# Performance work log

Measured on AMD Instinct MI355X. Metric: run time of the kernel, lower is better.

Reference implementation:

```python
import math
import jax, jax.numpy as jnp
import numpy as np

N, T, F, H = 30000, 4, 128, 8  # num_node, num_type, num_fea, num_head
D = F // H


def setup_inputs() -> dict:
    key = jax.random.key(0)
    k0, k1, k2, k3, k4 = jax.random.split(key, 5)
    feature = jax.random.normal(k0, (N, F), dtype=jnp.float32)
    edge_fea = jax.random.normal(k1, (N, T, F), dtype=jnp.float32)
    node_multi_mask = jax.random.randint(k2, (N,), 0, T)
    # Xavier-uniform-like scale for [*, F, F] projection tables
    xav = math.sqrt(6.0 / (F + F))
    node_proj = jax.random.uniform(k3, (T, F, F), minval=-xav, maxval=xav, dtype=jnp.float32)
    edge_proj = jax.random.uniform(k4, (T * T, F, F), minval=-xav, maxval=xav, dtype=jnp.float32)
    return {
        "feature": feature,
        "edge_fea": edge_fea,
        "node_multi_mask": node_multi_mask,
        "node_proj": node_proj,
        "edge_proj": edge_proj,
    }


def reference(feature, edge_fea, node_multi_mask, node_proj, edge_proj):
    # Type-indexed projections. Instead of gathering per-node [F,F] matrices
    # (which would materialize N*F*F), compute projections for all T source
    # types in one batched einsum, then select each node's type with a gather.
    # node: out[n] = node_proj[mask[n]] @ feature[n]
    node_all = jnp.einsum('tgf,nf->ntg', node_proj, feature)           # [N,T,F]
    node_p = jnp.take_along_axis(node_all, node_multi_mask[:, None, None], axis=1)[:, 0]  # [N,F]
    # edge: out[n,j] = edge_proj[mask[n]*T + j] @ edge_fea[n,j]
    edge_proj_r = edge_proj.reshape(T, T, F, F)                         # [src_type, j, F, F]
    edge_all = jnp.einsum('stgf,ntf->nstg', edge_proj_r, edge_fea)      # [N,T_src,T,F]
    edge_p = jnp.take_along_axis(edge_all, node_multi_mask[:, None, None, None], axis=1)[:, 0]  # [N,T,F]

    # multi-head attention weights
    node_multi_in = node_p.reshape(N, 1, H, D).transpose(0, 2, 1, 3) / math.sqrt(D)  # [N,H,1,D]
    edge_multi_in = edge_p.reshape(N, T, H, D).transpose(0, 2, 3, 1)                  # [N,H,D,T]
    scores = jnp.matmul(node_multi_in, edge_multi_in)                                 # [N,H,1,T]
    # NOTE: original uses nn.Softmax(dim=1) -> softmax over the HEAD axis
    all_r_weight = jax.nn.softmax(scores, axis=1).transpose(0, 3, 1, 2)               # [N,T,H,1]
    return all_r_weight
```

## Files before the change

### kernel.cpp

```cpp
#include <hip/hip_runtime.h>
#include <hip/hip_bf16.h>

#define N_NODES 30000
#define T_TYPES 4
#define F_DIM   128
#define H_HEADS 8

typedef __bf16 bf16x8 __attribute__((ext_vector_type(8)));
typedef __bf16 bf16x4 __attribute__((ext_vector_type(4)));
typedef float  floatx4 __attribute__((ext_vector_type(4)));

#define WS_REORDER 64
#define WS_NPB     480256
#define WS_EPB     611328

template <int CTRL>
static __device__ __forceinline__ float dpp_add(float x) {
    int xi = __builtin_bit_cast(int, x);
    int yi = __builtin_amdgcn_update_dpp(xi, xi, CTRL, 0xF, 0xF, true);
    return x + __builtin_bit_cast(float, yi);
}
static __device__ __forceinline__ float sum16(float x) {
    x = dpp_add<0xB1>(x);
    x = dpp_add<0x4E>(x);
    x = dpp_add<0x141>(x);
    x = dpp_add<0x140>(x);
    return x;
}

__global__ __launch_bounds__(256) void prep_kernel(
    const float* __restrict__ node_proj, const float* __restrict__ edge_proj,
    __bf16* __restrict__ npb, __bf16* __restrict__ epb, int* __restrict__ counts)
{
    int i = blockIdx.x * 256 + threadIdx.x;
    if (i < 4) counts[i] = 0;
    int base = i * 4;
    float4 v;
    __bf16* dst;
    if (base < T_TYPES * F_DIM * F_DIM) {
        v = ((const float4*)node_proj)[i];
        dst = npb + base;
    } else {
        int off = base - T_TYPES * F_DIM * F_DIM;
        v = ((const float4*)edge_proj)[off >> 2];
        dst = epb + off;
    }
    bf16x4 w = { (__bf16)v.x, (__bf16)v.y, (__bf16)v.z, (__bf16)v.w };
    *(bf16x4*)dst = w;
}

__global__ __launch_bounds__(256) void bucket_kernel(
    const int* __restrict__ mask, int* __restrict__ counts, int* __restrict__ reorder)
{
    int n = blockIdx.x * 256 + threadIdx.x;
    int lane = threadIdx.x & 63;
    int t = (n < N_NODES) ? mask[n] : -1;
    #pragma unroll
    for (int tt = 0; tt < T_TYPES; ++tt) {
        unsigned long long b = __ballot(t == tt);
        if (b == 0ull) continue;
        int cnt = __popcll(b);
        int leader = __ffsll((unsigned long long)b) - 1;
        int base = 0;
        if (lane == leader) base = atomicAdd(&counts[tt], cnt);
        base = __shfl(base, leader);
        if (t == tt) {
            int prefix = __popcll(b & ((1ull << lane) - 1ull));
            reorder[tt * N_NODES + base + prefix] = n;
        }
    }
}

__global__ __launch_bounds__(512) void main_kernel(
    const float* __restrict__ feature, const float* __restrict__ edge_fea,
    const int* __restrict__ counts, const int* __restrict__ reorder,
    const __bf16* __restrict__ npb, const __bf16* __restrict__ epb,
    float* __restrict__ out)
{
    const int b = blockIdx.x;
    const int t = b & 3;
    const int start = (b >> 2) * 32;
    const int Nt = counts[t];
    if (start >= Nt) return;
    const int valid = min(32, Nt - start);

    __shared__ __bf16 Afeat[32][136];
    __shared__ __bf16 Aedge[4][32][136];
    __shared__ float  sc[32][4][H_HEADS];
    __shared__ int    nidx[32];

    const int tid = threadIdx.x;
    if (tid < 32) {
        int s = (tid < valid) ? tid : (valid - 1);
        nidx[tid] = reorder[t * N_NODES + start + s];
    }
    __syncthreads();

    const int colv = tid & 31;
    const int rowg = tid >> 5;
    #pragma unroll
    for (int it = 0; it < 2; ++it) {
        int row = it * 16 + rowg;
        float4 v = ((const float4*)(feature + (long)nidx[row] * F_DIM))[colv];
        bf16x4 w = { (__bf16)v.x, (__bf16)v.y, (__bf16)v.z, (__bf16)v.w };
        *(bf16x4*)(&Afeat[row][0] + colv * 4) = w;
    }
    #pragma unroll
    for (int it = 0; it < 8; ++it) {
        int row = it * 16 + rowg;
        int j = row >> 5, r = row & 31;
        float4 v = ((const float4*)(edge_fea + ((long)nidx[r] * 4 + j) * F_DIM))[colv];
        bf16x4 w = { (__bf16)v.x, (__bf16)v.y, (__bf16)v.z, (__bf16)v.w };
        *(bf16x4*)(&Aedge[j][r][0] + colv * 4) = w;
    }
    __syncthreads();

    const int lane = tid & 63;
    const int wave = tid >> 6;
    const int ml   = lane & 15;
    const int quad = lane >> 4;
    const int g0   = wave * 16;

    floatx4 accN[2] = {};
    {
        const __bf16* a0 = &Afeat[ml][quad * 8];
        const __bf16* a1 = &Afeat[16 + ml][quad * 8];
        const __bf16* b0 = npb + t * (F_DIM * F_DIM) + (g0 + ml) * F_DIM + quad * 8;
        #pragma unroll
        for (int k0 = 0; k0 < 128; k0 += 32) {
            bf16x8 A0 = *(const bf16x8*)(a0 + k0);
            bf16x8 A1 = *(const bf16x8*)(a1 + k0);
            bf16x8 B0 = *(const bf16x8*)(b0 + k0);
            accN[0] = __builtin_amdgcn_mfma_f32_16x16x32_bf16(A0, B0, accN[0], 0, 0, 0);
            accN[1] = __builtin_amdgcn_mfma_f32_16x16x32_bf16(A1, B0, accN[1], 0, 0, 0);
        }
    }

    #pragma unroll
    for (int j = 0; j < 4; ++j) {
        floatx4 accE[2] = {};
        const __bf16* a0 = &Aedge[j][ml][quad * 8];
        const __bf16* a1 = &Aedge[j][16 + ml][quad * 8];
        const __bf16* b0 = epb + (t * 4 + j) * (F_DIM * F_DIM) + (g0 + ml) * F_DIM + quad * 8;
        #pragma unroll
        for (int k0 = 0; k0 < 128; k0 += 32) {
            bf16x8 A0 = *(const bf16x8*)(a0 + k0);
            bf16x8 A1 = *(const bf16x8*)(a1 + k0);
            bf16x8 B0 = *(const bf16x8*)(b0 + k0);
            accE[0] = __builtin_amdgcn_mfma_f32_16x16x32_bf16(A0, B0, accE[0], 0, 0, 0);
            accE[1] = __builtin_amdgcn_mfma_f32_16x16x32_bf16(A1, B0, accE[1], 0, 0, 0);
        }
        #pragma unroll
        for (int mt = 0; mt < 2; ++mt) {
            floatx4 p = accN[mt] * accE[mt];
            p.x = sum16(p.x);
            p.y = sum16(p.y);
            p.z = sum16(p.z);
            p.w = sum16(p.w);
            if (ml == 0) {
                int mb = mt * 16 + quad * 4;
                sc[mb + 0][j][wave] = p.x * 0.25f;
                sc[mb + 1][j][wave] = p.y * 0.25f;
                sc[mb + 2][j][wave] = p.z * 0.25f;
                sc[mb + 3][j][wave] = p.w * 0.25f;
            }
        }
    }
    __syncthreads();

    if (tid < 128) {
        int node = tid >> 2, j = tid & 3;
        if (node < valid) {
            float v[8], m = -1e30f;
            #pragma unroll
            for (int h = 0; h < 8; ++h) { v[h] = sc[node][j][h]; m = fmaxf(m, v[h]); }
            float s = 0.f;
            #pragma unroll
            for (int h = 0; h < 8; ++h) { v[h] = __expf(v[h] - m); s += v[h]; }
            float r = 1.0f / s;
            float* o = out + (long)nidx[node] * (T_TYPES * H_HEADS) + j * H_HEADS;
            float4 o0 = { v[0] * r, v[1] * r, v[2] * r, v[3] * r };
            float4 o1 = { v[4] * r, v[5] * r, v[6] * r, v[7] * r };
            ((float4*)o)[0] = o0;
            ((float4*)o)[1] = o1;
        }
    }
}

extern "C" void kernel_launch(void* const* d_in, const int* in_sizes, int n_in,
                              void* d_out, int out_size, void* d_ws, size_t ws_size,
                              hipStream_t stream) {
    const float* feature   = (const float*)d_in[0];
    const float* edge_fea  = (const float*)d_in[1];
    const int*   mask      = (const int*)d_in[2];
    const float* node_proj = (const float*)d_in[3];
    const float* edge_proj = (const float*)d_in[4];
    float* out = (float*)d_out;

    char* ws = (char*)d_ws;
    int*    counts  = (int*)ws;
    int*    reorder = (int*)(ws + WS_REORDER);
    __bf16* npb     = (__bf16*)(ws + WS_NPB);
    __bf16* epb     = (__bf16*)(ws + WS_EPB);

    prep_kernel<<<320, 256, 0, stream>>>(node_proj, edge_proj, npb, epb, counts);
    bucket_kernel<<<(N_NODES + 255) / 256, 256, 0, stream>>>(mask, counts, reorder);
    int nblk = ((N_NODES + 31) / 32) * T_TYPES;
    main_kernel<<<nblk, 512, 0, stream>>>(feature, edge_fea, counts, reorder, npb, epb, out);
}
```

Before: 144.9 us.

## Double-buffer edge tiles in LDS, merge prep and bucket kernels, raise occupancy

```diff
diff --git a/kernel.cpp b/kernel.cpp
--- a/kernel.cpp
+++ b/kernel.cpp
@@ -28,50 +28,49 @@
     return x;
 }
 
-__global__ __launch_bounds__(256) void prep_kernel(
+__global__ __launch_bounds__(256) void prep_bucket_kernel(
     const float* __restrict__ node_proj, const float* __restrict__ edge_proj,
-    __bf16* __restrict__ npb, __bf16* __restrict__ epb, int* __restrict__ counts)
+    const int* __restrict__ mask,
+    __bf16* __restrict__ npb, __bf16* __restrict__ epb,
+    int* __restrict__ counts, int* __restrict__ reorder)
 {
-    int i = blockIdx.x * 256 + threadIdx.x;
-    if (i < 4) counts[i] = 0;
-    int base = i * 4;
-    float4 v;
-    __bf16* dst;
-    if (base < T_TYPES * F_DIM * F_DIM) {
-        v = ((const float4*)node_proj)[i];
-        dst = npb + base;
+    if (blockIdx.x < 320) {
+        int i = blockIdx.x * 256 + threadIdx.x;
+        int base = i * 4;
+        float4 v;
+        __bf16* dst;
+        if (base < T_TYPES * F_DIM * F_DIM) {
+            v = ((const float4*)node_proj)[i];
+            dst = npb + base;
+        } else {
+            int off = base - T_TYPES * F_DIM * F_DIM;
+            v = ((const float4*)edge_proj)[off >> 2];
+            dst = epb + off;
+        }
+        bf16x4 w = { (__bf16)v.x, (__bf16)v.y, (__bf16)v.z, (__bf16)v.w };
+        *(bf16x4*)dst = w;
     } else {
-        int off = base - T_TYPES * F_DIM * F_DIM;
-        v = ((const float4*)edge_proj)[off >> 2];
-        dst = epb + off;
-    }
-    bf16x4 w = { (__bf16)v.x, (__bf16)v.y, (__bf16)v.z, (__bf16)v.w };
-    *(bf16x4*)dst = w;
-}
-
-__global__ __launch_bounds__(256) void bucket_kernel(
-    const int* __restrict__ mask, int* __restrict__ counts, int* __restrict__ reorder)
-{
-    int n = blockIdx.x * 256 + threadIdx.x;
-    int lane = threadIdx.x & 63;
-    int t = (n < N_NODES) ? mask[n] : -1;
-    #pragma unroll
-    for (int tt = 0; tt < T_TYPES; ++tt) {
-        unsigned long long b = __ballot(t == tt);
-        if (b == 0ull) continue;
-        int cnt = __popcll(b);
-        int leader = __ffsll((unsigned long long)b) - 1;
-        int base = 0;
-        if (lane == leader) base = atomicAdd(&counts[tt], cnt);
-        base = __shfl(base, leader);
-        if (t == tt) {
-            int prefix = __popcll(b & ((1ull << lane) - 1ull));
-            reorder[tt * N_NODES + base + prefix] = n;
-        }
-    }
-}
-
-__global__ __launch_bounds__(512) void main_kernel(
+        int n = (blockIdx.x - 320) * 256 + threadIdx.x;
+        int lane = threadIdx.x & 63;
+        int t = (n < N_NODES) ? mask[n] : -1;
+        #pragma unroll
+        for (int tt = 0; tt < T_TYPES; ++tt) {
+            unsigned long long b = __ballot(t == tt);
+            if (b == 0ull) continue;
+            int cnt = __popcll(b);
+            int leader = __ffsll((unsigned long long)b) - 1;
+            int base = 0;
+            if (lane == leader) base = atomicAdd(&counts[tt], cnt);
+            base = __shfl(base, leader);
+            if (t == tt) {
+                int prefix = __popcll(b & ((1ull << lane) - 1ull));
+                reorder[tt * N_NODES + base + prefix] = n;
+            }
+        }
+    }
+}
+
+__global__ __launch_bounds__(512, 8) void main_kernel(
     const float* __restrict__ feature, const float* __restrict__ edge_fea,
     const int* __restrict__ counts, const int* __restrict__ reorder,
     const __bf16* __restrict__ npb, const __bf16* __restrict__ epb,
@@ -85,7 +84,7 @@
     const int valid = min(32, Nt - start);
 
     __shared__ __bf16 Afeat[32][136];
-    __shared__ __bf16 Aedge[4][32][136];
+    __shared__ __bf16 Aedge[2][32][136];
     __shared__ float  sc[32][4][H_HEADS];
     __shared__ int    nidx[32];
 
@@ -98,20 +97,21 @@
 
     const int colv = tid & 31;
     const int rowg = tid >> 5;
-    #pragma unroll
-    for (int it = 0; it < 2; ++it) {
-        int row = it * 16 + rowg;
-        float4 v = ((const float4*)(feature + (long)nidx[row] * F_DIM))[colv];
-        bf16x4 w = { (__bf16)v.x, (__bf16)v.y, (__bf16)v.z, (__bf16)v.w };
-        *(bf16x4*)(&Afeat[row][0] + colv * 4) = w;
-    }
-    #pragma unroll
-    for (int it = 0; it < 8; ++it) {
-        int row = it * 16 + rowg;
-        int j = row >> 5, r = row & 31;
-        float4 v = ((const float4*)(edge_fea + ((long)nidx[r] * 4 + j) * F_DIM))[colv];
-        bf16x4 w = { (__bf16)v.x, (__bf16)v.y, (__bf16)v.z, (__bf16)v.w };
-        *(bf16x4*)(&Aedge[j][r][0] + colv * 4) = w;
+    const long nA = nidx[rowg], nB = nidx[rowg + 16];
+    {
+        float4 f0 = ((const float4*)(feature + nA * F_DIM))[colv];
+        float4 f1 = ((const float4*)(feature + nB * F_DIM))[colv];
+        float4 e0 = ((const float4*)(edge_fea + (nA * 4 + 0) * F_DIM))[colv];
+        float4 e1 = ((const float4*)(edge_fea + (nB * 4 + 0) * F_DIM))[colv];
+        bf16x4 w;
+        w = (bf16x4){ (__bf16)f0.x, (__bf16)f0.y, (__bf16)f0.z, (__bf16)f0.w };
+        *(bf16x4*)(&Afeat[rowg][0] + colv * 4) = w;
+        w = (bf16x4){ (__bf16)f1.x, (__bf16)f1.y, (__bf16)f1.z, (__bf16)f1.w };
+        *(bf16x4*)(&Afeat[rowg + 16][0] + colv * 4) = w;
+        w = (bf16x4){ (__bf16)e0.x, (__bf16)e0.y, (__bf16)e0.z, (__bf16)e0.w };
+        *(bf16x4*)(&Aedge[0][rowg][0] + colv * 4) = w;
+        w = (bf16x4){ (__bf16)e1.x, (__bf16)e1.y, (__bf16)e1.z, (__bf16)e1.w };
+        *(bf16x4*)(&Aedge[0][rowg + 16][0] + colv * 4) = w;
     }
     __syncthreads();
 
@@ -138,17 +138,24 @@
 
     #pragma unroll
     for (int j = 0; j < 4; ++j) {
+        float4 e0, e1;
+        if (j < 3) {
+            e0 = ((const float4*)(edge_fea + (nA * 4 + j + 1) * F_DIM))[colv];
+            e1 = ((const float4*)(edge_fea + (nB * 4 + j + 1) * F_DIM))[colv];
+        }
         floatx4 accE[2] = {};
-        const __bf16* a0 = &Aedge[j][ml][quad * 8];
-        const __bf16* a1 = &Aedge[j][16 + ml][quad * 8];
-        const __bf16* b0 = epb + (t * 4 + j) * (F_DIM * F_DIM) + (g0 + ml) * F_DIM + quad * 8;
-        #pragma unroll
-        for (int k0 = 0; k0 < 128; k0 += 32) {
-            bf16x8 A0 = *(const bf16x8*)(a0 + k0);
-            bf16x8 A1 = *(const bf16x8*)(a1 + k0);
-            bf16x8 B0 = *(const bf16x8*)(b0 + k0);
-            accE[0] = __builtin_amdgcn_mfma_f32_16x16x32_bf16(A0, B0, accE[0], 0, 0, 0);
-            accE[1] = __builtin_amdgcn_mfma_f32_16x16x32_bf16(A1, B0, accE[1], 0, 0, 0);
+        {
+            const __bf16* a0 = &Aedge[j & 1][ml][quad * 8];
+            const __bf16* a1 = &Aedge[j & 1][16 + ml][quad * 8];
+            const __bf16* b0 = epb + (t * 4 + j) * (F_DIM * F_DIM) + (g0 + ml) * F_DIM + quad * 8;
+            #pragma unroll
+            for (int k0 = 0; k0 < 128; k0 += 32) {
+                bf16x8 A0 = *(const bf16x8*)(a0 + k0);
+                bf16x8 A1 = *(const bf16x8*)(a1 + k0);
+                bf16x8 B0 = *(const bf16x8*)(b0 + k0);
+                accE[0] = __builtin_amdgcn_mfma_f32_16x16x32_bf16(A0, B0, accE[0], 0, 0, 0);
+                accE[1] = __builtin_amdgcn_mfma_f32_16x16x32_bf16(A1, B0, accE[1], 0, 0, 0);
+            }
         }
         #pragma unroll
         for (int mt = 0; mt < 2; ++mt) {
@@ -165,8 +172,15 @@
                 sc[mb + 3][j][wave] = p.w * 0.25f;
             }
         }
-    }
-    __syncthreads();
+        if (j < 3) {
+            bf16x4 w;
+            w = (bf16x4){ (__bf16)e0.x, (__bf16)e0.y, (__bf16)e0.z, (__bf16)e0.w };
+            *(bf16x4*)(&Aedge[(j + 1) & 1][rowg][0] + colv * 4) = w;
+            w = (bf16x4){ (__bf16)e1.x, (__bf16)e1.y, (__bf16)e1.z, (__bf16)e1.w };
+            *(bf16x4*)(&Aedge[(j + 1) & 1][rowg + 16][0] + colv * 4) = w;
+        }
+        __syncthreads();
+    }
 
     if (tid < 128) {
         int node = tid >> 2, j = tid & 3;
@@ -203,8 +217,9 @@
     __bf16* npb     = (__bf16*)(ws + WS_NPB);
     __bf16* epb     = (__bf16*)(ws + WS_EPB);
 
-    prep_kernel<<<320, 256, 0, stream>>>(node_proj, edge_proj, npb, epb, counts);
-    bucket_kernel<<<(N_NODES + 255) / 256, 256, 0, stream>>>(mask, counts, reorder);
+    hipMemsetAsync(counts, 0, 4 * sizeof(int), stream);
+    prep_bucket_kernel<<<320 + (N_NODES + 255) / 256, 256, 0, stream>>>(
+        node_proj, edge_proj, mask, npb, epb, counts, reorder);
     int nblk = ((N_NODES + 31) / 32) * T_TYPES;
     main_kernel<<<nblk, 512, 0, stream>>>(feature, edge_fea, counts, reorder, npb, epb, out);
 }
```

Result: no change. 146.9 us (+1.4%).
